# Performance work log

Measured on AMD Instinct MI355X. Metric: run time of the kernel, lower is better.

## Reference

```python
import jax, jax.numpy as jnp
import numpy as np

D_MODEL, WIN, STRIDE, NHEAD, HEAD_DIM, FFN_H = 96, 16, 8, 6, 16, 192
INNER = NHEAD * HEAD_DIM
EPS = 1e-5


def _ln(x, g, b):
    m = jnp.mean(x, axis=-1, keepdims=True)
    v = jnp.mean((x - m) ** 2, axis=-1, keepdims=True)
    return (x - m) / jnp.sqrt(v + EPS) * g + b


def setup_inputs() -> dict:
    key = jax.random.key(0)
    ks = jax.random.split(key, 16)
    B, L, D = 32, 8192, D_MODEL
    sd = lambda n: 1.0 / np.sqrt(n)
    return {
        "x": jax.random.normal(ks[0], (B, L, D), jnp.float32),
        "ln1_g": jnp.ones((D,), jnp.float32),
        "ln1_b": jnp.zeros((D,), jnp.float32),
        "qkv_w": jax.random.normal(ks[1], (D, 3 * INNER), jnp.float32) * sd(D),
        "qkv_b": jnp.zeros((3 * INNER,), jnp.float32),
        "out_w": jax.random.normal(ks[2], (INNER, D), jnp.float32) * sd(INNER),
        "out_b": jnp.zeros((D,), jnp.float32),
        "ln2_g": jnp.ones((D,), jnp.float32),
        "ln2_b": jnp.zeros((D,), jnp.float32),
        "ffn_w1": jax.random.normal(ks[3], (D, FFN_H), jnp.float32) * sd(D),
        "ffn_b1": jnp.zeros((FFN_H,), jnp.float32),
        "ffn_w2": jax.random.normal(ks[4], (FFN_H, D), jnp.float32) * sd(FFN_H),
        "ffn_b2": jnp.zeros((D,), jnp.float32),
        "pln_g": jnp.ones((D,), jnp.float32),
        "pln_b": jnp.zeros((D,), jnp.float32),
    }


def reference(x, ln1_g, ln1_b, qkv_w, qkv_b, out_w, out_b,
              ln2_g, ln2_b, ffn_w1, ffn_b1, ffn_w2, ffn_b2, pln_g, pln_b):
    B, L, D = x.shape
    w, s = WIN, STRIDE
    num_win = 1 + (L - w) // s  # all windows fit since (num_win-1)*s + w <= L
    idx = jnp.arange(num_win)[:, None] * s + jnp.arange(w)[None, :]  # [N, w]

    seg = x[:, idx]  # [B, N, w, D] gather of overlapping windows

    # --- pre-LN attention block, vectorized over all windows ---
    h = _ln(seg, ln1_g, ln1_b)
    qkv = h @ qkv_w + qkv_b  # [B, N, w, 3*INNER]
    q, k, v = jnp.split(qkv, 3, axis=-1)
    shp = (B, num_win, w, NHEAD, HEAD_DIM)
    q, k, v = q.reshape(shp), k.reshape(shp), v.reshape(shp)
    scores = jnp.einsum('bnqhd,bnkhd->bnhqk', q, k) / np.sqrt(HEAD_DIM).astype(np.float32)
    causal = jnp.tril(jnp.ones((w, w), bool))
    scores = jnp.where(causal, scores, -jnp.inf)
    attn = jax.nn.softmax(scores, axis=-1)
    o = jnp.einsum('bnhqk,bnkhd->bnqhd', attn, v).reshape(B, num_win, w, INNER)
    o = o @ out_w + out_b
    h = seg + o

    # --- FFN block ---
    h2 = _ln(h, ln2_g, ln2_b)
    h = h + (jax.nn.gelu(h2 @ ffn_w1 + ffn_b1) @ ffn_w2 + ffn_b2)
    h = _ln(h, pln_g, pln_b)

    # --- overlap-add average ---
    out = jnp.zeros((B, L, D), x.dtype).at[:, idx].add(h)
    cnt = jnp.zeros((L,), x.dtype).at[idx.reshape(-1)].add(1.0)
    return out / jnp.maximum(cnt, 1.0)[None, :, None]
```

## Files before the change

### kernel.cpp

```cpp
#include <hip/hip_runtime.h>
#include <hip/hip_bf16.h>

typedef __attribute__((ext_vector_type(8))) short short8;
typedef __attribute__((ext_vector_type(4))) float f32x4;

#define LDS_BYTES 50176

__device__ __forceinline__ unsigned short f2bf(float x){
  unsigned u = __float_as_uint(x);
  u += 0x7FFFu + ((u >> 16) & 1u);
  return (unsigned short)(u >> 16);
}

__global__ void pack_weights(const float* __restrict__ qkv_w, const float* __restrict__ out_w,
                             const float* __restrict__ ffn_w1, const float* __restrict__ ffn_w2,
                             short8* __restrict__ wsv){
  int f = blockIdx.x, lane = threadIdx.x;
  const float* W; int N, nt, kf;
  if (f < 54)      { W = qkv_w;  N = 288; nt = f/3;        kf = f%3; }
  else if (f < 72) { int i=f-54;  W = out_w;  N = 96;  nt = i/3; kf = i%3; }
  else if (f < 108){ int i=f-72;  W = ffn_w1; N = 192; nt = i/3; kf = i%3; }
  else             { int i=f-108; W = ffn_w2; N = 96;  nt = i/6; kf = i%6; }
  int n = lane & 15, kq = lane >> 4;
  short8 v;
#pragma unroll
  for (int j = 0; j < 8; ++j){
    int k = kf*32 + kq*8 + j;
    v[j] = (short)f2bf(W[(size_t)k * N + nt*16 + n]);
  }
  wsv[f*64 + lane] = v;
}

__global__ __launch_bounds__(512, 6)
void fused_block(const float* __restrict__ x,
                 const float* __restrict__ ln1_g, const float* __restrict__ ln1_b,
                 const float* __restrict__ qkv_b,
                 const float* __restrict__ out_b,
                 const float* __restrict__ ln2_g, const float* __restrict__ ln2_b,
                 const float* __restrict__ ffn_b1, const float* __restrict__ ffn_b2,
                 const float* __restrict__ pln_g, const float* __restrict__ pln_b,
                 const short8* __restrict__ wsv,
                 float* __restrict__ out)
{
  __shared__ __align__(16) char smem[LDS_BYTES];
  float*          hres = (float*)smem;
  unsigned short* Pb   = (unsigned short*)smem;
  unsigned short* buf1 = (unsigned short*)(smem + 19200);
  unsigned short* buf2 = (unsigned short*)(smem + 29184);

  const int tid  = threadIdx.x;
  const int wave = tid >> 6, lane = tid & 63;
  const int lm   = lane & 15, quad = lane >> 4;
  const int g = blockIdx.x, b = blockIdx.y;
  const int t0 = 24 * g;
  const size_t xbase = ((size_t)b * 8192 + t0) * 96;

  const int KOFF = 3328;
  const int VOFF = 6656;

  {
    const int row = tid >> 4, c0 = tid & 15;
    float v[6];
#pragma unroll
    for (int e = 0; e < 6; ++e) v[e] = x[xbase + (size_t)row*96 + c0 + 16*e];
    float s = 0.f, q2 = 0.f;
#pragma unroll
    for (int e = 0; e < 6; ++e){ s += v[e]; q2 += v[e]*v[e]; }
#pragma unroll
    for (int m = 1; m < 16; m <<= 1){ s += __shfl_xor(s, m, 16); q2 += __shfl_xor(q2, m, 16); }
    float mean = s * (1.f/96.f);
    float rstd = rsqrtf(q2 * (1.f/96.f) - mean*mean + 1e-5f);
#pragma unroll
    for (int e = 0; e < 6; ++e){
      int c = c0 + 16*e;
      buf1[row*104 + c] = f2bf((v[e] - mean) * rstd * ln1_g[c] + ln1_b[c]);
    }
  }
  __syncthreads();

  for (int tile = wave; tile < 36; tile += 8){
    int mt = tile & 1, nt = tile >> 1;
    f32x4 acc = {0.f,0.f,0.f,0.f};
#pragma unroll
    for (int kf = 0; kf < 3; ++kf){
      short8 a = *(const short8*)(buf1 + (16*mt + lm)*104 + kf*32 + quad*8);
      short8 w = wsv[(nt*3 + kf)*64 + lane];
      acc = __builtin_amdgcn_mfma_f32_16x16x32_bf16(a, w, acc, 0, 0, 0);
    }
    int col = nt*16 + lm;
    float bias = qkv_b[col];
    if (nt < 6){
#pragma unroll
      for (int r = 0; r < 4; ++r){
        int tok = 16*mt + quad*4 + r;
        buf2[tok*104 + col] = f2bf(acc[r] + bias);
      }
    } else if (nt < 12){
      int cl = col - 96;
#pragma unroll
      for (int r = 0; r < 4; ++r){
        int tok = 16*mt + quad*4 + r;
        buf2[KOFF + tok*104 + cl] = f2bf(acc[r] + bias);
      }
    } else {
      int d2 = col - 192;
#pragma unroll
      for (int r = 0; r < 4; ++r){
        int tok = 16*mt + quad*4 + r;
        buf2[VOFF + d2*40 + tok] = f2bf(acc[r] + bias);
      }
    }
  }
  __syncthreads();

  for (int u = wave; u < 18; u += 8){
    int w = u / 6, h = u % 6;
    short8 qa = {0,0,0,0,0,0,0,0}, ka = {0,0,0,0,0,0,0,0};
    if (quad < 2){
      qa = *(const short8*)(buf2 +        (8*w + lm)*104 + h*16 + quad*8);
      ka = *(const short8*)(buf2 + KOFF + (8*w + lm)*104 + h*16 + quad*8);
    }
    f32x4 sc = {0.f,0.f,0.f,0.f};
    sc = __builtin_amdgcn_mfma_f32_16x16x32_bf16(qa, ka, sc, 0, 0, 0);
#pragma unroll
    for (int r = 0; r < 4; ++r){
      int row = quad*4 + r;
      float s = (lm <= row) ? sc[r]*0.25f : -1e30f;
      float mx = s;
#pragma unroll
      for (int m = 1; m < 16; m <<= 1) mx = fmaxf(mx, __shfl_xor(mx, m, 16));
      float p = __expf(s - mx);
      float sum = p;
#pragma unroll
      for (int m = 1; m < 16; m <<= 1) sum += __shfl_xor(sum, m, 16);
      Pb[wave*384 + row*24 + lm] = f2bf(p / sum);
    }
    asm volatile("s_waitcnt lgkmcnt(0)" ::: "memory");
    short8 pa = {0,0,0,0,0,0,0,0}, va = {0,0,0,0,0,0,0,0};
    if (quad < 2){
      pa = *(const short8*)(Pb + wave*384 + lm*24 + quad*8);
      va = *(const short8*)(buf2 + VOFF + (h*16 + lm)*40 + 8*w + quad*8);
    }
    f32x4 oc = {0.f,0.f,0.f,0.f};
    oc = __builtin_amdgcn_mfma_f32_16x16x32_bf16(pa, va, oc, 0, 0, 0);
#pragma unroll
    for (int r = 0; r < 4; ++r)
      buf1[(w*16 + quad*4 + r)*104 + h*16 + lm] = f2bf(oc[r]);
  }
  __syncthreads();

  for (int tile = wave; tile < 18; tile += 8){
    int w = tile / 6, nt = tile % 6;
    f32x4 acc = {0.f,0.f,0.f,0.f};
#pragma unroll
    for (int kf = 0; kf < 3; ++kf){
      short8 a = *(const short8*)(buf1 + (w*16 + lm)*104 + kf*32 + quad*8);
      short8 wt = wsv[(54 + nt*3 + kf)*64 + lane];
      acc = __builtin_amdgcn_mfma_f32_16x16x32_bf16(a, wt, acc, 0, 0, 0);
    }
    int col = nt*16 + lm;
    float bias = out_b[col];
#pragma unroll
    for (int r = 0; r < 4; ++r){
      int i = quad*4 + r;
      float seg = x[xbase + (size_t)(8*w + i)*96 + col];
      hres[(w*16 + i)*100 + col] = acc[r] + bias + seg;
    }
  }
  __syncthreads();

  {
    const int r16 = tid >> 4, c0 = tid & 15;
#pragma unroll
    for (int p = 0; p < 2; ++p){
      int row = p*32 + r16;
      if (row < 48){
        float v[6];
#pragma unroll
        for (int e = 0; e < 6; ++e) v[e] = hres[row*100 + c0 + 16*e];
        float s = 0.f, q2 = 0.f;
#pragma unroll
        for (int e = 0; e < 6; ++e){ s += v[e]; q2 += v[e]*v[e]; }
#pragma unroll
        for (int m = 1; m < 16; m <<= 1){ s += __shfl_xor(s, m, 16); q2 += __shfl_xor(q2, m, 16); }
        float mean = s * (1.f/96.f);
        float rstd = rsqrtf(q2 * (1.f/96.f) - mean*mean + 1e-5f);
#pragma unroll
        for (int e = 0; e < 6; ++e){
          int c = c0 + 16*e;
          buf2[row*104 + c] = f2bf((v[e] - mean) * rstd * ln2_g[c] + ln2_b[c]);
        }
      }
    }
  }

  f32x4 facc0 = {0.f,0.f,0.f,0.f}, facc1 = {0.f,0.f,0.f,0.f}, facc2 = {0.f,0.f,0.f,0.f};
#pragma unroll
  for (int h = 0; h < 2; ++h){
    __syncthreads();
    for (int tile = wave; tile < 18; tile += 8){
      int mt = tile % 3, ntl = tile / 3;
      int ng = 6*h + ntl;
      f32x4 acc = {0.f,0.f,0.f,0.f};
#pragma unroll
      for (int kf = 0; kf < 3; ++kf){
        short8 a = *(const short8*)(buf2 + (mt*16 + lm)*104 + kf*32 + quad*8);
        short8 wt = wsv[(72 + ng*3 + kf)*64 + lane];
        acc = __builtin_amdgcn_mfma_f32_16x16x32_bf16(a, wt, acc, 0, 0, 0);
      }
      float bias = ffn_b1[ng*16 + lm];
#pragma unroll
      for (int r = 0; r < 4; ++r){
        float u = acc[r] + bias;
        float z = 0.7978845608f * (u + 0.044715f * u*u*u);
        z = fminf(fmaxf(z, -10.f), 10.f);
        float e2 = __expf(2.f * z);
        float th = (e2 - 1.f) / (e2 + 1.f);
        buf1[(mt*16 + quad*4 + r)*104 + ntl*16 + lm] = f2bf(0.5f * u * (1.f + th));
      }
    }
    __syncthreads();
    int s2 = 0;
    for (int tile = wave; tile < 18; tile += 8, ++s2){
      int mt = tile / 6, nt = tile % 6;
      f32x4 acc = (s2 == 0) ? facc0 : (s2 == 1) ? facc1 : facc2;
#pragma unroll
      for (int kf = 0; kf < 3; ++kf){
        short8 a = *(const short8*)(buf1 + (mt*16 + lm)*104 + kf*32 + quad*8);
        short8 wt = wsv[(108 + nt*6 + 3*h + kf)*64 + lane];
        acc = __builtin_amdgcn_mfma_f32_16x16x32_bf16(a, wt, acc, 0, 0, 0);
      }
      if (s2 == 0) facc0 = acc; else if (s2 == 1) facc1 = acc; else facc2 = acc;
    }
  }
  {
    int s2 = 0;
    for (int tile = wave; tile < 18; tile += 8, ++s2){
      int mt = tile / 6, nt = tile % 6;
      int col = nt*16 + lm;
      float bias = ffn_b2[col];
      f32x4 acc = (s2 == 0) ? facc0 : (s2 == 1) ? facc1 : facc2;
#pragma unroll
      for (int r = 0; r < 4; ++r)
        hres[(mt*16 + quad*4 + r)*100 + col] += acc[r] + bias;
    }
  }
  __syncthreads();

  {
    const int r16 = tid >> 4, c0 = tid & 15;
#pragma unroll
    for (int p = 0; p < 2; ++p){
      int row = p*32 + r16;
      if (row < 48){
        float v[6];
#pragma unroll
        for (int e = 0; e < 6; ++e) v[e] = hres[row*100 + c0 + 16*e];
        float s = 0.f, q2 = 0.f;
#pragma unroll
        for (int e = 0; e < 6; ++e){ s += v[e]; q2 += v[e]*v[e]; }
#pragma unroll
        for (int m = 1; m < 16; m <<= 1){ s += __shfl_xor(s, m, 16); q2 += __shfl_xor(q2, m, 16); }
        float mean = s * (1.f/96.f);
        float rstd = rsqrtf(q2 * (1.f/96.f) - mean*mean + 1e-5f);
#pragma unroll
        for (int e = 0; e < 6; ++e){
          int c = c0 + 16*e;
          hres[row*100 + c] = (v[e] - mean) * rstd * pln_g[c] + pln_b[c];
        }
      }
    }
  }
  __syncthreads();

  {
    const int i = tid >> 4, c0 = tid & 15;
    const int l = t0 + i;
    const size_t obase = ((size_t)b * 8192 + l) * 96;
    int rowA, rowB = -1;
    if (i < 8)       rowA = i;
    else if (i < 16){ rowA = i;            rowB = 16 + (i - 8);}
    else if (i < 24){ rowA = 16 + (i - 8); rowB = 32 + (i - 16);}
    else             rowA = 32 + (i - 16);
    if (rowB >= 0){
#pragma unroll
      for (int e = 0; e < 6; ++e){
        int c = c0 + 16*e;
        out[obase + c] = 0.5f * (hres[rowA*100 + c] + hres[rowB*100 + c]);
      }
    } else {
      float inv = (l < 8 || l >= 8184) ? 1.0f : 0.5f;
#pragma unroll
      for (int e = 0; e < 6; ++e){
        int c = c0 + 16*e;
        atomicAdd(&out[obase + c], hres[rowA*100 + c] * inv);
      }
    }
  }
}

extern "C" void kernel_launch(void* const* d_in, const int* in_sizes, int n_in,
                              void* d_out, int out_size, void* d_ws, size_t ws_size,
                              hipStream_t stream) {
  const float* x      = (const float*)d_in[0];
  const float* ln1_g  = (const float*)d_in[1];
  const float* ln1_b  = (const float*)d_in[2];
  const float* qkv_w  = (const float*)d_in[3];
  const float* qkv_b  = (const float*)d_in[4];
  const float* out_w  = (const float*)d_in[5];
  const float* out_b  = (const float*)d_in[6];
  const float* ln2_g  = (const float*)d_in[7];
  const float* ln2_b  = (const float*)d_in[8];
  const float* ffn_w1 = (const float*)d_in[9];
  const float* ffn_b1 = (const float*)d_in[10];
  const float* ffn_w2 = (const float*)d_in[11];
  const float* ffn_b2 = (const float*)d_in[12];
  const float* pln_g  = (const float*)d_in[13];
  const float* pln_b  = (const float*)d_in[14];
  float* out = (float*)d_out;
  short8* wsv = (short8*)d_ws;

  hipMemsetAsync(d_out, 0, (size_t)out_size * sizeof(float), stream);
  pack_weights<<<144, 64, 0, stream>>>(qkv_w, out_w, ffn_w1, ffn_w2, wsv);
  fused_block<<<dim3(341, 32), 512, 0, stream>>>(
      x, ln1_g, ln1_b, qkv_b, out_b, ln2_g, ln2_b, ffn_b1, ffn_b2,
      pln_g, pln_b, (const short8*)wsv, out);
}
```

Before: 479.3 us.

## Shrink LDS with bf16 residual, merge FFN passes, fuse final LN into overlap-add

```diff
diff --git a/kernel.cpp b/kernel.cpp
--- a/kernel.cpp
+++ b/kernel.cpp
@@ -4,13 +4,32 @@
 typedef __attribute__((ext_vector_type(8))) short short8;
 typedef __attribute__((ext_vector_type(4))) float f32x4;
 
-#define LDS_BYTES 50176
-
+#define LDS_BYTES 40960
+
+#if __has_builtin(__builtin_amdgcn_cvt_pk_bf16_f32)
+typedef __attribute__((ext_vector_type(2))) __bf16 bf16x2;
+__device__ __forceinline__ unsigned pk2bf(float a, float b){
+  bf16x2 v = __builtin_amdgcn_cvt_pk_bf16_f32(a, b);
+  return __builtin_bit_cast(unsigned, v);
+}
+__device__ __forceinline__ unsigned short f2bf(float x){
+  bf16x2 v = __builtin_amdgcn_cvt_pk_bf16_f32(x, x);
+  return (unsigned short)(__builtin_bit_cast(unsigned, v) & 0xFFFFu);
+}
+#else
 __device__ __forceinline__ unsigned short f2bf(float x){
   unsigned u = __float_as_uint(x);
   u += 0x7FFFu + ((u >> 16) & 1u);
   return (unsigned short)(u >> 16);
 }
+__device__ __forceinline__ unsigned pk2bf(float a, float b){
+  return (unsigned)f2bf(a) | ((unsigned)f2bf(b) << 16);
+}
+#endif
+
+__device__ __forceinline__ float bflo(unsigned u){ return __uint_as_float(u << 16); }
+__device__ __forceinline__ float bfhi(unsigned u){ return __uint_as_float(u & 0xFFFF0000u); }
+__device__ __forceinline__ float bf1(unsigned short h){ return __uint_as_float(((unsigned)h) << 16); }
 
 __global__ void pack_weights(const float* __restrict__ qkv_w, const float* __restrict__ out_w,
                              const float* __restrict__ ffn_w1, const float* __restrict__ ffn_w2,
@@ -31,7 +50,7 @@
   wsv[f*64 + lane] = v;
 }
 
-__global__ __launch_bounds__(512, 6)
+__global__ __launch_bounds__(512, 8)
 void fused_block(const float* __restrict__ x,
                  const float* __restrict__ ln1_g, const float* __restrict__ ln1_b,
                  const float* __restrict__ qkv_b,
@@ -43,10 +62,13 @@
                  float* __restrict__ out)
 {
   __shared__ __align__(16) char smem[LDS_BYTES];
-  float*          hres = (float*)smem;
-  unsigned short* Pb   = (unsigned short*)smem;
-  unsigned short* buf1 = (unsigned short*)(smem + 19200);
-  unsigned short* buf2 = (unsigned short*)(smem + 29184);
+  unsigned short* hres  = (unsigned short*)smem;
+  unsigned*       hresU = (unsigned*)smem;
+  unsigned short* Pb    = (unsigned short*)smem;
+  unsigned short* buf1  = (unsigned short*)(smem + 9984);
+  unsigned*       buf1U = (unsigned*)(smem + 9984);
+  unsigned short* buf2  = (unsigned short*)(smem + 19968);
+  unsigned*       buf2U = (unsigned*)(smem + 19968);
 
   const int tid  = threadIdx.x;
   const int wave = tid >> 6, lane = tid & 63;
@@ -59,10 +81,11 @@
   const int VOFF = 6656;
 
   {
-    const int row = tid >> 4, c0 = tid & 15;
+    const int row = tid >> 4, j = tid & 15;
+    const float* xr = x + xbase + (size_t)row*96 + 6*j;
     float v[6];
 #pragma unroll
-    for (int e = 0; e < 6; ++e) v[e] = x[xbase + (size_t)row*96 + c0 + 16*e];
+    for (int e = 0; e < 3; ++e){ float2 t = *(const float2*)(xr + 2*e); v[2*e]=t.x; v[2*e+1]=t.y; }
     float s = 0.f, q2 = 0.f;
 #pragma unroll
     for (int e = 0; e < 6; ++e){ s += v[e]; q2 += v[e]*v[e]; }
@@ -71,43 +94,42 @@
     float mean = s * (1.f/96.f);
     float rstd = rsqrtf(q2 * (1.f/96.f) - mean*mean + 1e-5f);
 #pragma unroll
-    for (int e = 0; e < 6; ++e){
-      int c = c0 + 16*e;
-      buf1[row*104 + c] = f2bf((v[e] - mean) * rstd * ln1_g[c] + ln1_b[c]);
-    }
-  }
-  __syncthreads();
-
-  for (int tile = wave; tile < 36; tile += 8){
-    int mt = tile & 1, nt = tile >> 1;
-    f32x4 acc = {0.f,0.f,0.f,0.f};
-#pragma unroll
-    for (int kf = 0; kf < 3; ++kf){
-      short8 a = *(const short8*)(buf1 + (16*mt + lm)*104 + kf*32 + quad*8);
-      short8 w = wsv[(nt*3 + kf)*64 + lane];
-      acc = __builtin_amdgcn_mfma_f32_16x16x32_bf16(a, w, acc, 0, 0, 0);
-    }
-    int col = nt*16 + lm;
-    float bias = qkv_b[col];
-    if (nt < 6){
-#pragma unroll
-      for (int r = 0; r < 4; ++r){
-        int tok = 16*mt + quad*4 + r;
-        buf2[tok*104 + col] = f2bf(acc[r] + bias);
-      }
-    } else if (nt < 12){
-      int cl = col - 96;
-#pragma unroll
-      for (int r = 0; r < 4; ++r){
-        int tok = 16*mt + quad*4 + r;
-        buf2[KOFF + tok*104 + cl] = f2bf(acc[r] + bias);
-      }
-    } else {
-      int d2 = col - 192;
-#pragma unroll
-      for (int r = 0; r < 4; ++r){
-        int tok = 16*mt + quad*4 + r;
-        buf2[VOFF + d2*40 + tok] = f2bf(acc[r] + bias);
+    for (int e = 0; e < 3; ++e){
+      float2 gg = *(const float2*)(ln1_g + 6*j + 2*e);
+      float2 bb = *(const float2*)(ln1_b + 6*j + 2*e);
+      buf1U[row*52 + 3*j + e] = pk2bf((v[2*e]-mean)*rstd*gg.x+bb.x,
+                                      (v[2*e+1]-mean)*rstd*gg.y+bb.y);
+    }
+  }
+  __syncthreads();
+
+  {
+    const int mt = wave & 1, p = wave >> 1;
+    const unsigned short* arow = buf1 + (16*mt + lm)*104 + quad*8;
+    short8 a0 = *(const short8*)(arow);
+    short8 a1 = *(const short8*)(arow + 32);
+    short8 a2 = *(const short8*)(arow + 64);
+    for (int nt = p; nt < 18; nt += 4){
+      f32x4 acc = {0.f,0.f,0.f,0.f};
+      acc = __builtin_amdgcn_mfma_f32_16x16x32_bf16(a0, wsv[(nt*3+0)*64 + lane], acc, 0, 0, 0);
+      acc = __builtin_amdgcn_mfma_f32_16x16x32_bf16(a1, wsv[(nt*3+1)*64 + lane], acc, 0, 0, 0);
+      acc = __builtin_amdgcn_mfma_f32_16x16x32_bf16(a2, wsv[(nt*3+2)*64 + lane], acc, 0, 0, 0);
+      int col = nt*16 + lm;
+      float bias = qkv_b[col];
+      if (nt < 6){
+#pragma unroll
+        for (int r = 0; r < 4; ++r)
+          buf2[(16*mt + quad*4 + r)*104 + col] = f2bf(acc[r] + bias);
+      } else if (nt < 12){
+        int cl = col - 96;
+#pragma unroll
+        for (int r = 0; r < 4; ++r)
+          buf2[KOFF + (16*mt + quad*4 + r)*104 + cl] = f2bf(acc[r] + bias);
+      } else {
+        int d2 = col - 192;
+        int w0 = (VOFF >> 1) + d2*20 + 8*mt + 2*quad;
+        buf2U[w0]     = pk2bf(acc[0] + bias, acc[1] + bias);
+        buf2U[w0 + 1] = pk2bf(acc[2] + bias, acc[3] + bias);
       }
     }
   }
@@ -155,29 +177,31 @@
 #pragma unroll
     for (int kf = 0; kf < 3; ++kf){
       short8 a = *(const short8*)(buf1 + (w*16 + lm)*104 + kf*32 + quad*8);
-      short8 wt = wsv[(54 + nt*3 + kf)*64 + lane];
-      acc = __builtin_amdgcn_mfma_f32_16x16x32_bf16(a, wt, acc, 0, 0, 0);
+      acc = __builtin_amdgcn_mfma_f32_16x16x32_bf16(a, wsv[(54 + nt*3 + kf)*64 + lane], acc, 0, 0, 0);
     }
     int col = nt*16 + lm;
     float bias = out_b[col];
 #pragma unroll
     for (int r = 0; r < 4; ++r){
-      int i = quad*4 + r;
-      float seg = x[xbase + (size_t)(8*w + i)*96 + col];
-      hres[(w*16 + i)*100 + col] = acc[r] + bias + seg;
+      int i2 = quad*4 + r;
+      float seg = x[xbase + (size_t)(8*w + i2)*96 + col];
+      hres[(w*16 + i2)*104 + col] = f2bf(acc[r] + bias + seg);
     }
   }
   __syncthreads();
 
   {
-    const int r16 = tid >> 4, c0 = tid & 15;
+    const int j = tid & 15;
 #pragma unroll
     for (int p = 0; p < 2; ++p){
-      int row = p*32 + r16;
+      int row = p*32 + (tid >> 4);
       if (row < 48){
         float v[6];
 #pragma unroll
-        for (int e = 0; e < 6; ++e) v[e] = hres[row*100 + c0 + 16*e];
+        for (int e = 0; e < 3; ++e){
+          unsigned u = hresU[row*52 + 3*j + e];
+          v[2*e] = bflo(u); v[2*e+1] = bfhi(u);
+        }
         float s = 0.f, q2 = 0.f;
 #pragma unroll
         for (int e = 0; e < 6; ++e){ s += v[e]; q2 += v[e]*v[e]; }
@@ -186,115 +210,122 @@
         float mean = s * (1.f/96.f);
         float rstd = rsqrtf(q2 * (1.f/96.f) - mean*mean + 1e-5f);
 #pragma unroll
-        for (int e = 0; e < 6; ++e){
-          int c = c0 + 16*e;
-          buf2[row*104 + c] = f2bf((v[e] - mean) * rstd * ln2_g[c] + ln2_b[c]);
+        for (int e = 0; e < 3; ++e){
+          float2 gg = *(const float2*)(ln2_g + 6*j + 2*e);
+          float2 bb = *(const float2*)(ln2_b + 6*j + 2*e);
+          buf1U[row*52 + 3*j + e] = pk2bf((v[2*e]-mean)*rstd*gg.x+bb.x,
+                                          (v[2*e+1]-mean)*rstd*gg.y+bb.y);
         }
       }
     }
   }
-
-  f32x4 facc0 = {0.f,0.f,0.f,0.f}, facc1 = {0.f,0.f,0.f,0.f}, facc2 = {0.f,0.f,0.f,0.f};
-#pragma unroll
-  for (int h = 0; h < 2; ++h){
-    __syncthreads();
-    for (int tile = wave; tile < 18; tile += 8){
-      int mt = tile % 3, ntl = tile / 3;
-      int ng = 6*h + ntl;
-      f32x4 acc = {0.f,0.f,0.f,0.f};
-#pragma unroll
-      for (int kf = 0; kf < 3; ++kf){
-        short8 a = *(const short8*)(buf2 + (mt*16 + lm)*104 + kf*32 + quad*8);
-        short8 wt = wsv[(72 + ng*3 + kf)*64 + lane];
-        acc = __builtin_amdgcn_mfma_f32_16x16x32_bf16(a, wt, acc, 0, 0, 0);
-      }
-      float bias = ffn_b1[ng*16 + lm];
-#pragma unroll
-      for (int r = 0; r < 4; ++r){
-        float u = acc[r] + bias;
-        float z = 0.7978845608f * (u + 0.044715f * u*u*u);
-        z = fminf(fmaxf(z, -10.f), 10.f);
-        float e2 = __expf(2.f * z);
-        float th = (e2 - 1.f) / (e2 + 1.f);
-        buf1[(mt*16 + quad*4 + r)*104 + ntl*16 + lm] = f2bf(0.5f * u * (1.f + th));
-      }
-    }
-    __syncthreads();
-    int s2 = 0;
-    for (int tile = wave; tile < 18; tile += 8, ++s2){
-      int mt = tile / 6, nt = tile % 6;
-      f32x4 acc = (s2 == 0) ? facc0 : (s2 == 1) ? facc1 : facc2;
-#pragma unroll
-      for (int kf = 0; kf < 3; ++kf){
-        short8 a = *(const short8*)(buf1 + (mt*16 + lm)*104 + kf*32 + quad*8);
-        short8 wt = wsv[(108 + nt*6 + 3*h + kf)*64 + lane];
-        acc = __builtin_amdgcn_mfma_f32_16x16x32_bf16(a, wt, acc, 0, 0, 0);
-      }
-      if (s2 == 0) facc0 = acc; else if (s2 == 1) facc1 = acc; else facc2 = acc;
-    }
-  }
+  __syncthreads();
+
+  for (int tile = wave; tile < 36; tile += 8){
+    int mt = tile % 3, nt = tile / 3;
+    f32x4 acc = {0.f,0.f,0.f,0.f};
+#pragma unroll
+    for (int kf = 0; kf < 3; ++kf){
+      short8 a = *(const short8*)(buf1 + (mt*16 + lm)*104 + kf*32 + quad*8);
+      acc = __builtin_amdgcn_mfma_f32_16x16x32_bf16(a, wsv[(72 + nt*3 + kf)*64 + lane], acc, 0, 0, 0);
+    }
+    float bias = ffn_b1[nt*16 + lm];
+#pragma unroll
+    for (int r = 0; r < 4; ++r){
+      float u = acc[r] + bias;
+      float z = 0.7978845608f * (u + 0.044715f * u*u*u);
+      z = fminf(fmaxf(z, -10.f), 10.f);
+      float e2 = __expf(2.f * z);
+      float th = (e2 - 1.f) / (e2 + 1.f);
+      buf2[(mt*16 + quad*4 + r)*200 + nt*16 + lm] = f2bf(0.5f * u * (1.f + th));
+    }
+  }
+  __syncthreads();
+
+  for (int tile = wave; tile < 18; tile += 8){
+    int mt = tile / 6, nt = tile % 6;
+    f32x4 acc = {0.f,0.f,0.f,0.f};
+#pragma unroll
+    for (int kf = 0; kf < 6; ++kf){
+      short8 a = *(const short8*)(buf2 + (mt*16 + lm)*200 + kf*32 + quad*8);
+      acc = __builtin_amdgcn_mfma_f32_16x16x32_bf16(a, wsv[(108 + nt*6 + kf)*64 + lane], acc, 0, 0, 0);
+    }
+    int col = nt*16 + lm;
+    float bias = ffn_b2[col];
+#pragma unroll
+    for (int r = 0; r < 4; ++r){
+      int idx = (mt*16 + quad*4 + r)*104 + col;
+      hres[idx] = f2bf(bf1(hres[idx]) + acc[r] + bias);
+    }
+  }
+  __syncthreads();
+
   {
-    int s2 = 0;
-    for (int tile = wave; tile < 18; tile += 8, ++s2){
-      int mt = tile / 6, nt = tile % 6;
-      int col = nt*16 + lm;
-      float bias = ffn_b2[col];
-      f32x4 acc = (s2 == 0) ? facc0 : (s2 == 1) ? facc1 : facc2;
-#pragma unroll
-      for (int r = 0; r < 4; ++r)
-        hres[(mt*16 + quad*4 + r)*100 + col] += acc[r] + bias;
-    }
-  }
-  __syncthreads();
-
-  {
-    const int r16 = tid >> 4, c0 = tid & 15;
-#pragma unroll
-    for (int p = 0; p < 2; ++p){
-      int row = p*32 + r16;
-      if (row < 48){
-        float v[6];
-#pragma unroll
-        for (int e = 0; e < 6; ++e) v[e] = hres[row*100 + c0 + 16*e];
-        float s = 0.f, q2 = 0.f;
-#pragma unroll
-        for (int e = 0; e < 6; ++e){ s += v[e]; q2 += v[e]*v[e]; }
-#pragma unroll
-        for (int m = 1; m < 16; m <<= 1){ s += __shfl_xor(s, m, 16); q2 += __shfl_xor(q2, m, 16); }
-        float mean = s * (1.f/96.f);
-        float rstd = rsqrtf(q2 * (1.f/96.f) - mean*mean + 1e-5f);
-#pragma unroll
-        for (int e = 0; e < 6; ++e){
-          int c = c0 + 16*e;
-          hres[row*100 + c] = (v[e] - mean) * rstd * pln_g[c] + pln_b[c];
-        }
-      }
-    }
-  }
-  __syncthreads();
-
-  {
-    const int i = tid >> 4, c0 = tid & 15;
+    const int i = tid >> 4, j = tid & 15;
     const int l = t0 + i;
     const size_t obase = ((size_t)b * 8192 + l) * 96;
     int rowA, rowB = -1;
     if (i < 8)       rowA = i;
-    else if (i < 16){ rowA = i;            rowB = 16 + (i - 8);}
-    else if (i < 24){ rowA = 16 + (i - 8); rowB = 32 + (i - 16);}
+    else if (i < 16){ rowA = i;            rowB = 16 + (i - 8); }
+    else if (i < 24){ rowA = 16 + (i - 8); rowB = 32 + (i - 16); }
     else             rowA = 32 + (i - 16);
+
+    float g6[6], b6[6];
+#pragma unroll
+    for (int e = 0; e < 3; ++e){
+      float2 gv = *(const float2*)(pln_g + 6*j + 2*e);
+      float2 bv = *(const float2*)(pln_b + 6*j + 2*e);
+      g6[2*e] = gv.x; g6[2*e+1] = gv.y; b6[2*e] = bv.x; b6[2*e+1] = bv.y;
+    }
+    float yA[6];
+    {
+      float v[6];
+#pragma unroll
+      for (int e = 0; e < 3; ++e){
+        unsigned u = hresU[rowA*52 + 3*j + e];
+        v[2*e] = bflo(u); v[2*e+1] = bfhi(u);
+      }
+      float s = 0.f, q2 = 0.f;
+#pragma unroll
+      for (int e = 0; e < 6; ++e){ s += v[e]; q2 += v[e]*v[e]; }
+#pragma unroll
+      for (int m = 1; m < 16; m <<= 1){ s += __shfl_xor(s, m, 16); q2 += __shfl_xor(q2, m, 16); }
+      float mean = s * (1.f/96.f);
+      float rstd = rsqrtf(q2 * (1.f/96.f) - mean*mean + 1e-5f);
+#pragma unroll
+      for (int e = 0; e < 6; ++e) yA[e] = (v[e]-mean)*rstd*g6[e] + b6[e];
+    }
     if (rowB >= 0){
-#pragma unroll
-      for (int e = 0; e < 6; ++e){
-        int c = c0 + 16*e;
-        out[obase + c] = 0.5f * (hres[rowA*100 + c] + hres[rowB*100 + c]);
+      float yB[6];
+      {
+        float v[6];
+#pragma unroll
+        for (int e = 0; e < 3; ++e){
+          unsigned u = hresU[rowB*52 + 3*j + e];
+          v[2*e] = bflo(u); v[2*e+1] = bfhi(u);
+        }
+        float s = 0.f, q2 = 0.f;
+#pragma unroll
+        for (int e = 0; e < 6; ++e){ s += v[e]; q2 += v[e]*v[e]; }
+#pragma unroll
+        for (int m = 1; m < 16; m <<= 1){ s += __shfl_xor(s, m, 16); q2 += __shfl_xor(q2, m, 16); }
+        float mean = s * (1.f/96.f);
+        float rstd = rsqrtf(q2 * (1.f/96.f) - mean*mean + 1e-5f);
+#pragma unroll
+        for (int e = 0; e < 6; ++e) yB[e] = (v[e]-mean)*rstd*g6[e] + b6[e];
+      }
+#pragma unroll
+      for (int e = 0; e < 3; ++e){
+        float2 o2;
+        o2.x = 0.5f * (yA[2*e]   + yB[2*e]);
+        o2.y = 0.5f * (yA[2*e+1] + yB[2*e+1]);
+        *(float2*)(out + obase + 6*j + 2*e) = o2;
       }
     } else {
       float inv = (l < 8 || l >= 8184) ? 1.0f : 0.5f;
 #pragma unroll
-      for (int e = 0; e < 6; ++e){
-        int c = c0 + 16*e;
-        atomicAdd(&out[obase + c], hres[rowA*100 + c] * inv);
-      }
+      for (int e = 0; e < 6; ++e)
+        atomicAdd(&out[obase + 6*j + e], yA[e] * inv);
     }
   }
 }
```

Result: slower. 530.6 us (+10.7%).
